# Kernel optimization log

Hardware: AMD Instinct MI355X
Metric: run time of the kernel (lower is better)

## Reference

```python
import jax, jax.numpy as jnp
import numpy as np

B, S, D, H = 4, 2048, 512, 8
DH = D // H  # 64


def setup_inputs() -> dict:
    key = jax.random.key(0)
    ks = jax.random.split(key, 12)
    sc = 0.02
    return {
        "embed": jax.random.normal(ks[0], (B, S, D), dtype=jnp.float32),
        "Wq": jax.random.normal(ks[1], (H, DH, D), dtype=jnp.float32) * sc,
        "bq": jax.random.normal(ks[2], (H, DH), dtype=jnp.float32) * sc,
        "Wk": jax.random.normal(ks[3], (H, DH, D), dtype=jnp.float32) * sc,
        "bk": jax.random.normal(ks[4], (H, DH), dtype=jnp.float32) * sc,
        "Wv": jax.random.normal(ks[5], (H, DH, D), dtype=jnp.float32) * sc,
        "bv": jax.random.normal(ks[6], (H, DH), dtype=jnp.float32) * sc,
        "Wo": jax.random.normal(ks[7], (D, D), dtype=jnp.float32) * sc,
        "bo": jax.random.normal(ks[8], (D,), dtype=jnp.float32) * sc,
        "gamma": jnp.ones((D,), dtype=jnp.float32),
        "beta": jnp.zeros((D,), dtype=jnp.float32),
    }


def reference(embed, Wq, bq, Wk, bk, Wv, bv, Wo, bo, gamma, beta):
    # Per-head linear projections, vectorized over heads: [B,H,S,DH]
    q = jnp.einsum("bsd,hed->bhse", embed, Wq) + bq[None, :, None, :]
    k = jnp.einsum("bsd,hed->bhse", embed, Wk) + bk[None, :, None, :]
    v = jnp.einsum("bsd,hed->bhse", embed, Wv) + bv[None, :, None, :]

    # Full score matrix [B,H,S,S], tril applied to RAW scores (zeros, not -inf),
    # scaled by sqrt(embedding_dim) -- faithful to the original module's math.
    att = jnp.einsum("bhse,bhte->bhst", q, k)
    att = jnp.tril(att)
    att = att / jnp.sqrt(jnp.float32(D))
    att = jax.nn.softmax(att, axis=-1)

    out = jnp.einsum("bhst,bhte->bhse", att, v)  # [B,H,S,DH]
    # concat heads along feature dim -> [B,S,D]
    out = jnp.transpose(out, (0, 2, 1, 3)).reshape(B, S, D)

    x = out @ Wo.T + bo
    x = x + embed

    # LayerNorm over last dim
    mu = jnp.mean(x, axis=-1, keepdims=True)
    var = jnp.var(x, axis=-1, keepdims=True)
    x = (x - mu) / jnp.sqrt(var + 1e-5) * gamma + beta
    return x
```

## Files before the change

### kernel.cpp

```cpp
#include <hip/hip_runtime.h>
#include <hip/hip_bf16.h>


typedef __bf16 bf16;
typedef __bf16 bf16x8 __attribute__((ext_vector_type(8)));
typedef __bf16 bf16x4v __attribute__((ext_vector_type(4)));
typedef float f32x4 __attribute__((ext_vector_type(4)));

#define S_LEN 2048
#define DMODEL 512
#define QSCALE 0.06375870914f

#define GLDS(g, l) __builtin_amdgcn_global_load_lds(                  \
    (const __attribute__((address_space(1))) void*)(g),               \
    (__attribute__((address_space(3))) void*)(l), 16, 0, 0)

__global__ __launch_bounds__(256) void cast_all(
    const float* __restrict__ embed, const float* __restrict__ Wq,
    const float* __restrict__ Wk, const float* __restrict__ Wv,
    const float* __restrict__ Wo,
    bf16* __restrict__ Eb, bf16* __restrict__ Wqkv, bf16* __restrict__ Wob) {
  int i = blockIdx.x * 256 + threadIdx.x;
  const float* src;
  bf16* dst;
  int il;
  if (i < 1048576) {
    src = embed; dst = Eb; il = i;
  } else {
    int j = i - 1048576;
    int w = j >> 16;
    il = j & 65535;
    src = (w == 0) ? Wq : (w == 1) ? Wk : (w == 2) ? Wv : Wo;
    dst = (w == 3) ? Wob : Wqkv + (size_t)w * 262144;
  }
  float4 v = reinterpret_cast<const float4*>(src)[il];
  bf16x4v o;
  o[0] = (bf16)v.x; o[1] = (bf16)v.y; o[2] = (bf16)v.z; o[3] = (bf16)v.w;
  *reinterpret_cast<bf16x4v*>(dst + (size_t)il * 4) = o;
}

__device__ __forceinline__ void gemm128_core(
    const bf16* __restrict__ A, const bf16* __restrict__ Bw,
    int row0, int col0, bf16* As, bf16* Bs, f32x4 (&acc)[4][4]) {
  int tid = threadIdx.x;
  int w = tid >> 6, l = tid & 63, lr = l & 15, lg = l >> 4;
  int wr = w >> 1, wc = w & 1;

  int srow = w * 8 + (l >> 3);
  int scol = ((l & 7) ^ (srow & 7)) << 3;
  const bf16* ga = A + (size_t)(row0 + srow) * DMODEL + scol;
  const bf16* gb = Bw + (size_t)(col0 + srow) * DMODEL + scol;
  char* asb = (char*)As;
  char* bsb = (char*)Bs;
  int sbase = w * 1024;

  int aoff[4], boff[4];
#pragma unroll
  for (int m = 0; m < 4; ++m) {
    aoff[m] = (wr * 64 + m * 16 + lr) * 128 + (((lg ^ (lr & 7))) << 4);
    boff[m] = (wc * 64 + m * 16 + lr) * 128 + (((lg ^ (lr & 7))) << 4);
  }

  for (int k0 = 0; k0 < DMODEL; k0 += 64) {
#pragma unroll
    for (int qt = 0; qt < 4; ++qt) {
      GLDS(ga + (size_t)qt * 32 * DMODEL, asb + qt * 4096 + sbase);
      GLDS(gb + (size_t)qt * 32 * DMODEL, bsb + qt * 4096 + sbase);
    }
    ga += 64; gb += 64;
    __syncthreads();

    bf16x8 af[2][4], bfv[2][4];
#pragma unroll
    for (int m = 0; m < 4; ++m) {
      af[0][m] = *(const bf16x8*)(asb + aoff[m]);
      af[1][m] = *(const bf16x8*)(asb + (aoff[m] ^ 0x40));
      bfv[0][m] = *(const bf16x8*)(bsb + boff[m]);
      bfv[1][m] = *(const bf16x8*)(bsb + (boff[m] ^ 0x40));
    }
#pragma unroll
    for (int m = 0; m < 4; ++m)
#pragma unroll
      for (int n = 0; n < 4; ++n) {
        acc[m][n] = __builtin_amdgcn_mfma_f32_16x16x32_bf16(af[0][m], bfv[0][n], acc[m][n], 0, 0, 0);
        acc[m][n] = __builtin_amdgcn_mfma_f32_16x16x32_bf16(af[1][m], bfv[1][n], acc[m][n], 0, 0, 0);
      }
    __syncthreads();
  }
}

__global__ __launch_bounds__(256) void gemm_qkv(
    const bf16* __restrict__ A, const bf16* __restrict__ Wqkv,
    const float* __restrict__ bq, const float* __restrict__ bk, const float* __restrict__ bv,
    bf16* __restrict__ Qb, bf16* __restrict__ Kb, bf16* __restrict__ Vt) {
  __shared__ __align__(16) bf16 As[128 * 64];
  __shared__ __align__(16) bf16 Bs[128 * 64];
  int row0 = blockIdx.x * 128, col0 = blockIdx.y * 128;
  f32x4 acc[4][4] = {};
  gemm128_core(A, Wqkv, row0, col0, As, Bs, acc);

  int tid = threadIdx.x;
  int w = tid >> 6, l = tid & 63, lr = l & 15, lg = l >> 4;
  int wr = w >> 1, wc = w & 1;
  int z2 = col0 >> 9;
  if (z2 < 2) {
    bf16* O = z2 ? Kb : Qb;
    const float* bias = z2 ? bk : bq;
    float qs = z2 ? 1.0f : QSCALE;
#pragma unroll
    for (int n = 0; n < 4; ++n) {
      int cg = (col0 & 511) + wc * 64 + n * 16 + lr;
      float bi = bias[cg];
#pragma unroll
      for (int m = 0; m < 4; ++m) {
        int rg = row0 + wr * 64 + m * 16 + lg * 4;
#pragma unroll
        for (int r = 0; r < 4; ++r)
          O[(size_t)(rg + r) * DMODEL + cg] = (bf16)((acc[m][n][r] + bi) * qs);
      }
    }
  } else {
#pragma unroll
    for (int n = 0; n < 4; ++n) {
      int ep = (col0 & 511) + wc * 64 + n * 16 + lr;
      int h = ep >> 6, e = ep & 63;
      float bi = bv[ep];
#pragma unroll
      for (int m = 0; m < 4; ++m) {
        int rg = row0 + wr * 64 + m * 16 + lg * 4;
        int b = rg >> 11, s0 = rg & 2047;
        bf16x4v pk;
#pragma unroll
        for (int r = 0; r < 4; ++r) pk[r] = (bf16)(acc[m][n][r] + bi);
        *(bf16x4v*)(Vt + ((size_t)((b * 8 + h) * 64 + e)) * S_LEN + s0) = pk;
      }
    }
  }
}

__global__ __launch_bounds__(256) void gemm_wo(
    const bf16* __restrict__ A, const bf16* __restrict__ W,
    const float* __restrict__ bo, const float* __restrict__ embed,
    bf16* __restrict__ X) {
  __shared__ __align__(16) bf16 As[128 * 64];
  __shared__ __align__(16) bf16 Bs[128 * 64];
  int row0 = blockIdx.x * 128, col0 = blockIdx.y * 128;
  f32x4 acc[4][4] = {};
  gemm128_core(A, W, row0, col0, As, Bs, acc);

  int tid = threadIdx.x;
  int w = tid >> 6, l = tid & 63, lr = l & 15, lg = l >> 4;
  int wr = w >> 1, wc = w & 1;
#pragma unroll
  for (int n = 0; n < 4; ++n) {
    int cg = col0 + wc * 64 + n * 16 + lr;
    float bi = bo[cg];
#pragma unroll
    for (int m = 0; m < 4; ++m) {
      int rg = row0 + wr * 64 + m * 16 + lg * 4;
#pragma unroll
      for (int r = 0; r < 4; ++r)
        X[(size_t)(rg + r) * DMODEL + cg] =
            (bf16)(acc[m][n][r] + bi + embed[(size_t)(rg + r) * DMODEL + cg]);
    }
  }
}

__global__ __launch_bounds__(512) void suf_kernel(const bf16* __restrict__ Vt,
                                                  float* __restrict__ SUF) {
  int bh = blockIdx.x;
  int e = threadIdx.x & 63;
  int seg = threadIdx.x >> 6;
  __shared__ float segtot[8][64];
  const bf16* vrow = Vt + ((size_t)bh * 64 + e) * S_LEN;
  float loc[16];
  float carry = 0.f;
#pragma unroll
  for (int j = 15; j >= 0; --j) {
    int jj = seg * 16 + j;
    bf16x8 a = *(const bf16x8*)(vrow + jj * 16);
    bf16x8 b2 = *(const bf16x8*)(vrow + jj * 16 + 8);
    float s = 0.f;
#pragma unroll
    for (int k = 0; k < 8; ++k) s += (float)a[k] + (float)b2[k];
    carry += s;
    loc[j] = carry;
  }
  segtot[seg][e] = carry;
  __syncthreads();
  float add = 0.f;
  for (int s2 = seg + 1; s2 < 8; ++s2) add += segtot[s2][e];
  float* srow = SUF + (size_t)bh * 129 * 64 + e;
#pragma unroll
  for (int j = 0; j < 16; ++j) srow[(size_t)(seg * 16 + j) * 64] = loc[j] + add;
  if (threadIdx.x < 64) srow[(size_t)128 * 64] = 0.f;
}

__global__ __launch_bounds__(512) void flash_attn(
    const bf16* __restrict__ Qb, const bf16* __restrict__ Kb,
    const bf16* __restrict__ Vt, const float* __restrict__ SUF,
    bf16* __restrict__ attO) {
  int bh = blockIdx.y;
  int b = bh >> 3, h = bh & 7;
  int p = (int)gridDim.x - 1 - (int)blockIdx.x;
  int tid = threadIdx.x;
  int w = tid >> 6, l = tid & 63, lr = l & 15, lg = l >> 4;
  int wsub = w & 3;
  int qtile = (w < 4) ? (16 + p) : (15 - p);
  int qb = qtile * 64;
  int nt = 17 + p;

  __shared__ __align__(16) bf16 kl[2][64 * 64];
  __shared__ __align__(16) bf16 vl[2][64 * 64];
  __shared__ __align__(16) bf16 pl[8][16 * 64];

  int srow = qb + 16 * wsub + lr;
  const bf16* qptr = Qb + ((size_t)(b * S_LEN) + srow) * DMODEL + h * 64 + lg * 8;
  bf16x8 aq0 = *(const bf16x8*)(qptr);
  bf16x8 aq1 = *(const bf16x8*)(qptr + 32);

  float lsum[4] = {0.f, 0.f, 0.f, 0.f};
  f32x4 acc[4] = {};

  int tmax_w = qb + 16 * wsub + 16;

  int grow = tid >> 3, gch = tid & 7;
  int sch = ((gch ^ (grow & 7)) << 3);
  const bf16* Kg = Kb + ((size_t)(b * S_LEN) + grow) * DMODEL + h * 64 + sch;
  const bf16* Vg = Vt + ((size_t)(bh * 64) + grow) * S_LEN + sch;
  int sdst = w * 1024;

  int sw0 = (lg ^ (lr & 7)) << 4;
  int sw4 = sw0 ^ 0x40;
  char* plb = (char*)pl[w];

  GLDS(Kg, (char*)kl[0] + sdst);
  GLDS(Vg, (char*)vl[0] + sdst);
  asm volatile("s_waitcnt vmcnt(0)" ::: "memory");
  __syncthreads();

  int cur = 0;
  for (int it = 0; it < nt; ++it) {
    int t0 = it << 6;
    if (it + 1 < nt) {
      GLDS(Kg + (size_t)(t0 + 64) * DMODEL, (char*)kl[cur ^ 1] + sdst);
      GLDS(Vg + (t0 + 64), (char*)vl[cur ^ 1] + sdst);
    }
    if (t0 < tmax_w) {
      char* klb = (char*)kl[cur];
      char* vlb = (char*)vl[cur];

      f32x4 sfrag[4];
      const f32x4 fz = {0.f, 0.f, 0.f, 0.f};
      __builtin_amdgcn_s_setprio(1);
#pragma unroll
      for (int c = 0; c < 4; ++c) {
        int rb = (16 * c + lr) * 128;
        bf16x8 bk0 = *(const bf16x8*)(klb + rb + sw0);
        bf16x8 bk1 = *(const bf16x8*)(klb + rb + sw4);
        f32x4 t = __builtin_amdgcn_mfma_f32_16x16x32_bf16(aq0, bk0, fz, 0, 0, 0);
        sfrag[c] = __builtin_amdgcn_mfma_f32_16x16x32_bf16(aq1, bk1, t, 0, 0, 0);
      }
      __builtin_amdgcn_s_setprio(0);

      if (t0 + 64 <= qb + 16 * wsub) {
#pragma unroll
        for (int r = 0; r < 4; ++r) {
          int row = lg * 4 + r;
          int pbase = row * 128 + ((lr & 7) << 1);
          int xorv = row & 7;
          float psum = 0.f;
#pragma unroll
          for (int c = 0; c < 4; ++c) {
            float pv = exp2f(sfrag[c][r]);
            psum += pv;
            int chunk = 2 * c + (lr >> 3);
            *(bf16*)(plb + pbase + (((chunk ^ xorv) << 4))) = (bf16)pv;
          }
          lsum[r] += psum;
        }
      } else {
#pragma unroll
        for (int r = 0; r < 4; ++r) {
          int sg = qb + 16 * wsub + lg * 4 + r;
          int row = lg * 4 + r;
          int pbase = row * 128 + ((lr & 7) << 1);
          int xorv = row & 7;
          float psum = 0.f;
#pragma unroll
          for (int c = 0; c < 4; ++c) {
            int tg = t0 + 16 * c + lr;
            float x = (tg <= sg) ? sfrag[c][r] : ((tg < tmax_w) ? 0.f : -1e30f);
            float pv = exp2f(x);
            psum += pv;
            int chunk = 2 * c + (lr >> 3);
            *(bf16*)(plb + pbase + (((chunk ^ xorv) << 4))) = (bf16)pv;
          }
          lsum[r] += psum;
        }
      }

      bf16x8 pa0 = *(const bf16x8*)(plb + lr * 128 + sw0);
      bf16x8 pa1 = *(const bf16x8*)(plb + lr * 128 + sw4);
      __builtin_amdgcn_s_setprio(1);
#pragma unroll
      for (int c = 0; c < 4; ++c) {
        int rb = (16 * c + lr) * 128;
        bf16x8 bv0 = *(const bf16x8*)(vlb + rb + sw0);
        bf16x8 bv1 = *(const bf16x8*)(vlb + rb + sw4);
        acc[c] = __builtin_amdgcn_mfma_f32_16x16x32_bf16(pa0, bv0, acc[c], 0, 0, 0);
        acc[c] = __builtin_amdgcn_mfma_f32_16x16x32_bf16(pa1, bv1, acc[c], 0, 0, 0);
      }
      __builtin_amdgcn_s_setprio(0);
    }
    asm volatile("s_waitcnt vmcnt(0)" ::: "memory");
    __syncthreads();
    cur ^= 1;
  }

#pragma unroll
  for (int r = 0; r < 4; ++r) {
#pragma unroll
    for (int d = 1; d < 16; d <<= 1) lsum[r] += __shfl_xor(lsum[r], d, 64);
  }

  int j16 = tmax_w >> 4;
  const float* suf = SUF + ((size_t)bh * 129 + j16) * 64;
  float cnt = (float)(S_LEN - tmax_w);
  float sufe[4];
#pragma unroll
  for (int c = 0; c < 4; ++c) sufe[c] = suf[16 * c + lr];
#pragma unroll
  for (int r = 0; r < 4; ++r) {
    float inv = 1.f / (lsum[r] + cnt);
    int sg = qb + 16 * wsub + lg * 4 + r;
#pragma unroll
    for (int c = 0; c < 4; ++c) {
      float o = (acc[c][r] + sufe[c]) * inv;
      attO[((size_t)(b * S_LEN) + sg) * DMODEL + h * 64 + 16 * c + lr] = (bf16)o;
    }
  }
}

__global__ __launch_bounds__(256) void ln_kernel(const bf16* __restrict__ x,
                                                 const float* __restrict__ gamma,
                                                 const float* __restrict__ beta,
                                                 float* __restrict__ out) {
  int row = blockIdx.x * 4 + (threadIdx.x >> 6);
  int l = threadIdx.x & 63;
  bf16x8 xv = *(const bf16x8*)(x + (size_t)row * DMODEL + l * 8);
  float xf[8];
  float s = 0.f, s2 = 0.f;
#pragma unroll
  for (int k = 0; k < 8; ++k) {
    xf[k] = (float)xv[k];
    s += xf[k];
    s2 += xf[k] * xf[k];
  }
#pragma unroll
  for (int d = 1; d < 64; d <<= 1) {
    s += __shfl_xor(s, d, 64);
    s2 += __shfl_xor(s2, d, 64);
  }
  float mean = s * (1.f / 512.f);
  float var = s2 * (1.f / 512.f) - mean * mean;
  float rstd = rsqrtf(var + 1e-5f);
  const float4* g4 = reinterpret_cast<const float4*>(gamma) + l * 2;
  const float4* b4 = reinterpret_cast<const float4*>(beta) + l * 2;
  float4 g0 = g4[0], g1 = g4[1], bb0 = b4[0], bb1 = b4[1];
  float4 o0, o1;
  o0.x = (xf[0] - mean) * rstd * g0.x + bb0.x;
  o0.y = (xf[1] - mean) * rstd * g0.y + bb0.y;
  o0.z = (xf[2] - mean) * rstd * g0.z + bb0.z;
  o0.w = (xf[3] - mean) * rstd * g0.w + bb0.w;
  o1.x = (xf[4] - mean) * rstd * g1.x + bb1.x;
  o1.y = (xf[5] - mean) * rstd * g1.y + bb1.y;
  o1.z = (xf[6] - mean) * rstd * g1.z + bb1.z;
  o1.w = (xf[7] - mean) * rstd * g1.w + bb1.w;
  float4* orow = reinterpret_cast<float4*>(out + (size_t)row * DMODEL) + l * 2;
  orow[0] = o0;
  orow[1] = o1;
}

extern "C" void kernel_launch(void* const* d_in, const int* in_sizes, int n_in,
                              void* d_out, int out_size, void* d_ws, size_t ws_size,
                              hipStream_t stream) {
  const float* embed = (const float*)d_in[0];
  const float* Wq = (const float*)d_in[1];
  const float* bq = (const float*)d_in[2];
  const float* Wk = (const float*)d_in[3];
  const float* bk = (const float*)d_in[4];
  const float* Wv = (const float*)d_in[5];
  const float* bv = (const float*)d_in[6];
  const float* Wo = (const float*)d_in[7];
  const float* bo = (const float*)d_in[8];
  const float* gamma = (const float*)d_in[9];
  const float* beta = (const float*)d_in[10];
  float* out = (float*)d_out;

  char* ws = (char*)d_ws;
  size_t off = 0;
  auto alc = [&](size_t b) { size_t o = off; off += (b + 255) & ~(size_t)255; return o; };
  bf16* Eb    = (bf16*)(ws + alc(8192ull * 512 * 2));
  bf16* Wqkv  = (bf16*)(ws + alc(1536ull * 512 * 2));
  bf16* Wob   = (bf16*)(ws + alc(512ull * 512 * 2));
  bf16* Qb    = (bf16*)(ws + alc(8192ull * 512 * 2));
  bf16* Kb    = (bf16*)(ws + alc(8192ull * 512 * 2));
  bf16* Vt    = (bf16*)(ws + alc(8192ull * 512 * 2));
  float* SUF  = (float*)(ws + alc(32ull * 129 * 64 * 4));
  bf16* AttO  = (bf16*)(ws + alc(8192ull * 512 * 2));
  bf16* Xb    = (bf16*)(ws + alc(8192ull * 512 * 2));
  (void)ws_size; (void)n_in; (void)in_sizes; (void)out_size;

  cast_all<<<5120, 256, 0, stream>>>(embed, Wq, Wk, Wv, Wo, Eb, Wqkv, Wob);

  gemm_qkv<<<dim3(64, 12), 256, 0, stream>>>(Eb, Wqkv, bq, bk, bv, Qb, Kb, Vt);
  suf_kernel<<<32, 512, 0, stream>>>(Vt, SUF);
  flash_attn<<<dim3(16, 32), 512, 0, stream>>>(Qb, Kb, Vt, SUF, AttO);
  gemm_wo<<<dim3(64, 4), 256, 0, stream>>>(AttO, Wob, bo, embed, Xb);
  ln_kernel<<<2048, 256, 0, stream>>>(Xb, gamma, beta, out);
}
```

Measured before the change: 111.3 us.

## Use 32x32x16 MFMA with register-resident P via permlane swaps in attention

Rewrites the flash attention inner loop to compute S^T with 32x32x16 MFMAs, so each wave owns 32 query rows. The P matrix now stays in registers, rearranged with v_permlane32_swap, which removes the per-wave LDS staging of P and the extra LDS round trips. Blocks are reassigned so each handles 4 pairs of 32-row tiles (front and back) over 8 x-blocks, with per-wave early cutoff and diagonal masking at 32-row granularity. The row sums are reduced through a small shared array for output normalisation. The cost is fewer blocks and more accumulator registers per wave.

```diff
diff --git a/kernel.cpp b/kernel.cpp
--- a/kernel.cpp
+++ b/kernel.cpp
@@ -5,7 +5,11 @@
 typedef __bf16 bf16;
 typedef __bf16 bf16x8 __attribute__((ext_vector_type(8)));
 typedef __bf16 bf16x4v __attribute__((ext_vector_type(4)));
+typedef __bf16 bf16x2 __attribute__((ext_vector_type(2)));
 typedef float f32x4 __attribute__((ext_vector_type(4)));
+typedef float f32x16 __attribute__((ext_vector_type(16)));
+typedef unsigned int u32;
+typedef u32 u32x4 __attribute__((ext_vector_type(4)));
 
 #define S_LEN 2048
 #define DMODEL 512
@@ -14,6 +18,8 @@
 #define GLDS(g, l) __builtin_amdgcn_global_load_lds(                  \
     (const __attribute__((address_space(1))) void*)(g),               \
     (__attribute__((address_space(3))) void*)(l), 16, 0, 0)
+
+#define PSWAP(a, b) asm volatile("v_permlane32_swap_b32 %0, %1" : "+v"(a), "+v"(b))
 
 __global__ __launch_bounds__(256) void cast_all(
     const float* __restrict__ embed, const float* __restrict__ Wq,
@@ -196,33 +202,54 @@
   if (threadIdx.x < 64) srow[(size_t)128 * 64] = 0.f;
 }
 
+__device__ __forceinline__ void softmax_pack(const f32x16& sf, bool diag, int lh,
+                                             int ls, float& lsum, u32* w8) {
+#pragma unroll
+  for (int i = 0; i < 8; ++i) {
+    float x0 = sf[2 * i], x1 = sf[2 * i + 1];
+    if (diag) {
+      int t0 = ((2 * i) & 3) + 8 * (i >> 1) + 4 * lh;
+      x0 = (t0 <= ls) ? x0 : 0.f;
+      x1 = (t0 + 1 <= ls) ? x1 : 0.f;
+    }
+    float e0 = exp2f(x0), e1 = exp2f(x1);
+    lsum += e0 + e1;
+    bf16x2 pk;
+    pk[0] = (bf16)e0; pk[1] = (bf16)e1;
+    w8[i] = __builtin_bit_cast(u32, pk);
+  }
+}
+
 __global__ __launch_bounds__(512) void flash_attn(
     const bf16* __restrict__ Qb, const bf16* __restrict__ Kb,
     const bf16* __restrict__ Vt, const float* __restrict__ SUF,
     bf16* __restrict__ attO) {
   int bh = blockIdx.y;
   int b = bh >> 3, h = bh & 7;
-  int p = (int)gridDim.x - 1 - (int)blockIdx.x;
+  int p = blockIdx.x;
   int tid = threadIdx.x;
-  int w = tid >> 6, l = tid & 63, lr = l & 15, lg = l >> 4;
+  int w = tid >> 6, l = tid & 63, lh = l >> 5, ls = l & 31;
+
+  int pe = (w >> 2) ? (p + 8) : p;
   int wsub = w & 3;
-  int qtile = (w < 4) ? (16 + p) : (15 - p);
-  int qb = qtile * 64;
-  int nt = 17 + p;
+  int qt32 = (wsub < 2) ? (32 + 2 * pe + wsub) : (31 - 2 * pe - (wsub - 2));
+  int qb_w = qt32 * 32;
+  int tmax_w = qb_w + 32;
+  int nt_w = (tmax_w + 63) >> 6;
+  int nt = 25 + p;
+  int dsub = (qb_w >> 5) & 1;
 
   __shared__ __align__(16) bf16 kl[2][64 * 64];
   __shared__ __align__(16) bf16 vl[2][64 * 64];
-  __shared__ __align__(16) bf16 pl[8][16 * 64];
-
-  int srow = qb + 16 * wsub + lr;
-  const bf16* qptr = Qb + ((size_t)(b * S_LEN) + srow) * DMODEL + h * 64 + lg * 8;
-  bf16x8 aq0 = *(const bf16x8*)(qptr);
-  bf16x8 aq1 = *(const bf16x8*)(qptr + 32);
-
-  float lsum[4] = {0.f, 0.f, 0.f, 0.f};
-  f32x4 acc[4] = {};
-
-  int tmax_w = qb + 16 * wsub + 16;
+  __shared__ float lsumS[8][32];
+
+  const bf16* qrow = Qb + ((size_t)(b * S_LEN) + qb_w + ls) * DMODEL + h * 64 + lh * 8;
+  bf16x8 qf[4];
+#pragma unroll
+  for (int ki = 0; ki < 4; ++ki) qf[ki] = *(const bf16x8*)(qrow + ki * 16);
+
+  f32x16 acc0 = {}, acc1 = {};
+  float lsum = 0.f;
 
   int grow = tid >> 3, gch = tid & 7;
   int sch = ((gch ^ (grow & 7)) << 3);
@@ -230,9 +257,10 @@
   const bf16* Vg = Vt + ((size_t)(bh * 64) + grow) * S_LEN + sch;
   int sdst = w * 1024;
 
-  int sw0 = (lg ^ (lr & 7)) << 4;
-  int sw4 = sw0 ^ 0x40;
-  char* plb = (char*)pl[w];
+  int cx[4];
+#pragma unroll
+  for (int ki = 0; ki < 4; ++ki) cx[ki] = (((2 * ki + lh) ^ (ls & 7)) << 4);
+  int rb = ls * 128;
 
   GLDS(Kg, (char*)kl[0] + sdst);
   GLDS(Vg, (char*)vl[0] + sdst);
@@ -241,104 +269,90 @@
 
   int cur = 0;
   for (int it = 0; it < nt; ++it) {
-    int t0 = it << 6;
     if (it + 1 < nt) {
-      GLDS(Kg + (size_t)(t0 + 64) * DMODEL, (char*)kl[cur ^ 1] + sdst);
-      GLDS(Vg + (t0 + 64), (char*)vl[cur ^ 1] + sdst);
-    }
-    if (t0 < tmax_w) {
+      int t1 = (it + 1) << 6;
+      GLDS(Kg + (size_t)t1 * DMODEL, (char*)kl[cur ^ 1] + sdst);
+      GLDS(Vg + t1, (char*)vl[cur ^ 1] + sdst);
+    }
+    if (it < nt_w) {
       char* klb = (char*)kl[cur];
       char* vlb = (char*)vl[cur];
-
-      f32x4 sfrag[4];
-      const f32x4 fz = {0.f, 0.f, 0.f, 0.f};
-      __builtin_amdgcn_s_setprio(1);
-#pragma unroll
-      for (int c = 0; c < 4; ++c) {
-        int rb = (16 * c + lr) * 128;
-        bf16x8 bk0 = *(const bf16x8*)(klb + rb + sw0);
-        bf16x8 bk1 = *(const bf16x8*)(klb + rb + sw4);
-        f32x4 t = __builtin_amdgcn_mfma_f32_16x16x32_bf16(aq0, bk0, fz, 0, 0, 0);
-        sfrag[c] = __builtin_amdgcn_mfma_f32_16x16x32_bf16(aq1, bk1, t, 0, 0, 0);
-      }
-      __builtin_amdgcn_s_setprio(0);
-
-      if (t0 + 64 <= qb + 16 * wsub) {
-#pragma unroll
-        for (int r = 0; r < 4; ++r) {
-          int row = lg * 4 + r;
-          int pbase = row * 128 + ((lr & 7) << 1);
-          int xorv = row & 7;
-          float psum = 0.f;
-#pragma unroll
-          for (int c = 0; c < 4; ++c) {
-            float pv = exp2f(sfrag[c][r]);
-            psum += pv;
-            int chunk = 2 * c + (lr >> 3);
-            *(bf16*)(plb + pbase + (((chunk ^ xorv) << 4))) = (bf16)pv;
-          }
-          lsum[r] += psum;
+      bool last = (it == nt_w - 1);
+      int nsub = (last && dsub == 0) ? 1 : 2;
+
+      f32x16 sf0 = {}, sf1 = {};
+#pragma unroll
+      for (int ki = 0; ki < 4; ++ki) {
+        bf16x8 ka = *(const bf16x8*)(klb + rb + cx[ki]);
+        sf0 = __builtin_amdgcn_mfma_f32_32x32x16_bf16(ka, qf[ki], sf0, 0, 0, 0);
+      }
+      if (nsub == 2) {
+#pragma unroll
+        for (int ki = 0; ki < 4; ++ki) {
+          bf16x8 ka = *(const bf16x8*)(klb + rb + 32 * 128 + cx[ki]);
+          sf1 = __builtin_amdgcn_mfma_f32_32x32x16_bf16(ka, qf[ki], sf1, 0, 0, 0);
         }
-      } else {
-#pragma unroll
-        for (int r = 0; r < 4; ++r) {
-          int sg = qb + 16 * wsub + lg * 4 + r;
-          int row = lg * 4 + r;
-          int pbase = row * 128 + ((lr & 7) << 1);
-          int xorv = row & 7;
-          float psum = 0.f;
-#pragma unroll
-          for (int c = 0; c < 4; ++c) {
-            int tg = t0 + 16 * c + lr;
-            float x = (tg <= sg) ? sfrag[c][r] : ((tg < tmax_w) ? 0.f : -1e30f);
-            float pv = exp2f(x);
-            psum += pv;
-            int chunk = 2 * c + (lr >> 3);
-            *(bf16*)(plb + pbase + (((chunk ^ xorv) << 4))) = (bf16)pv;
-          }
-          lsum[r] += psum;
-        }
-      }
-
-      bf16x8 pa0 = *(const bf16x8*)(plb + lr * 128 + sw0);
-      bf16x8 pa1 = *(const bf16x8*)(plb + lr * 128 + sw4);
-      __builtin_amdgcn_s_setprio(1);
-#pragma unroll
-      for (int c = 0; c < 4; ++c) {
-        int rb = (16 * c + lr) * 128;
-        bf16x8 bv0 = *(const bf16x8*)(vlb + rb + sw0);
-        bf16x8 bv1 = *(const bf16x8*)(vlb + rb + sw4);
-        acc[c] = __builtin_amdgcn_mfma_f32_16x16x32_bf16(pa0, bv0, acc[c], 0, 0, 0);
-        acc[c] = __builtin_amdgcn_mfma_f32_16x16x32_bf16(pa1, bv1, acc[c], 0, 0, 0);
-      }
-      __builtin_amdgcn_s_setprio(0);
+      }
+
+      u32 pw[16];
+      softmax_pack(sf0, last && (dsub == 0), lh, ls, lsum, pw);
+      PSWAP(pw[0], pw[2]); PSWAP(pw[1], pw[3]);
+      PSWAP(pw[4], pw[6]); PSWAP(pw[5], pw[7]);
+      if (nsub == 2) {
+        softmax_pack(sf1, last && (dsub == 1), lh, ls, lsum, pw + 8);
+        PSWAP(pw[8], pw[10]); PSWAP(pw[9], pw[11]);
+        PSWAP(pw[12], pw[14]); PSWAP(pw[13], pw[15]);
+      }
+
+      u32x4 f0v = {pw[0], pw[1], pw[2], pw[3]};
+      u32x4 f1v = {pw[4], pw[5], pw[6], pw[7]};
+      bf16x8 pa0 = __builtin_bit_cast(bf16x8, f0v);
+      bf16x8 pa1 = __builtin_bit_cast(bf16x8, f1v);
+      {
+        bf16x8 v00 = *(const bf16x8*)(vlb + rb + cx[0]);
+        bf16x8 v01 = *(const bf16x8*)(vlb + rb + cx[1]);
+        bf16x8 v10 = *(const bf16x8*)(vlb + rb + 32 * 128 + cx[0]);
+        bf16x8 v11 = *(const bf16x8*)(vlb + rb + 32 * 128 + cx[1]);
+        acc0 = __builtin_amdgcn_mfma_f32_32x32x16_bf16(pa0, v00, acc0, 0, 0, 0);
+        acc0 = __builtin_amdgcn_mfma_f32_32x32x16_bf16(pa1, v01, acc0, 0, 0, 0);
+        acc1 = __builtin_amdgcn_mfma_f32_32x32x16_bf16(pa0, v10, acc1, 0, 0, 0);
+        acc1 = __builtin_amdgcn_mfma_f32_32x32x16_bf16(pa1, v11, acc1, 0, 0, 0);
+      }
+      if (nsub == 2) {
+        u32x4 f2v = {pw[8], pw[9], pw[10], pw[11]};
+        u32x4 f3v = {pw[12], pw[13], pw[14], pw[15]};
+        bf16x8 pa2 = __builtin_bit_cast(bf16x8, f2v);
+        bf16x8 pa3 = __builtin_bit_cast(bf16x8, f3v);
+        bf16x8 v02 = *(const bf16x8*)(vlb + rb + cx[2]);
+        bf16x8 v03 = *(const bf16x8*)(vlb + rb + cx[3]);
+        bf16x8 v12 = *(const bf16x8*)(vlb + rb + 32 * 128 + cx[2]);
+        bf16x8 v13 = *(const bf16x8*)(vlb + rb + 32 * 128 + cx[3]);
+        acc0 = __builtin_amdgcn_mfma_f32_32x32x16_bf16(pa2, v02, acc0, 0, 0, 0);
+        acc0 = __builtin_amdgcn_mfma_f32_32x32x16_bf16(pa3, v03, acc0, 0, 0, 0);
+        acc1 = __builtin_amdgcn_mfma_f32_32x32x16_bf16(pa2, v12, acc1, 0, 0, 0);
+        acc1 = __builtin_amdgcn_mfma_f32_32x32x16_bf16(pa3, v13, acc1, 0, 0, 0);
+      }
     }
     asm volatile("s_waitcnt vmcnt(0)" ::: "memory");
     __syncthreads();
     cur ^= 1;
   }
 
-#pragma unroll
-  for (int r = 0; r < 4; ++r) {
-#pragma unroll
-    for (int d = 1; d < 16; d <<= 1) lsum[r] += __shfl_xor(lsum[r], d, 64);
-  }
+  lsum += __shfl_xor(lsum, 32, 64);
+  lsumS[w][ls] = lsum;
 
   int j16 = tmax_w >> 4;
   const float* suf = SUF + ((size_t)bh * 129 + j16) * 64;
   float cnt = (float)(S_LEN - tmax_w);
-  float sufe[4];
-#pragma unroll
-  for (int c = 0; c < 4; ++c) sufe[c] = suf[16 * c + lr];
-#pragma unroll
-  for (int r = 0; r < 4; ++r) {
-    float inv = 1.f / (lsum[r] + cnt);
-    int sg = qb + 16 * wsub + lg * 4 + r;
-#pragma unroll
-    for (int c = 0; c < 4; ++c) {
-      float o = (acc[c][r] + sufe[c]) * inv;
-      attO[((size_t)(b * S_LEN) + sg) * DMODEL + h * 64 + 16 * c + lr] = (bf16)o;
-    }
+  float suf0 = suf[ls], suf1 = suf[ls + 32];
+
+  bf16* obase = attO + ((size_t)(b * S_LEN) + qb_w) * DMODEL + h * 64 + ls;
+#pragma unroll
+  for (int r = 0; r < 16; ++r) {
+    int sr = (r & 3) + 8 * (r >> 2) + 4 * lh;
+    float inv = 1.f / (lsumS[w][sr] + cnt);
+    obase[(size_t)sr * DMODEL] = (bf16)((acc0[r] + suf0) * inv);
+    obase[(size_t)sr * DMODEL + 32] = (bf16)((acc1[r] + suf1) * inv);
   }
 }
 
@@ -416,7 +430,7 @@
 
   gemm_qkv<<<dim3(64, 12), 256, 0, stream>>>(Eb, Wqkv, bq, bk, bv, Qb, Kb, Vt);
   suf_kernel<<<32, 512, 0, stream>>>(Vt, SUF);
-  flash_attn<<<dim3(16, 32), 512, 0, stream>>>(Qb, Kb, Vt, SUF, AttO);
+  flash_attn<<<dim3(8, 32), 512, 0, stream>>>(Qb, Kb, Vt, SUF, AttO);
   gemm_wo<<<dim3(64, 4), 256, 0, stream>>>(AttO, Wob, bo, embed, Xb);
   ln_kernel<<<2048, 256, 0, stream>>>(Xb, gamma, beta, out);
 }
```

Measured after the change: 128.3 us. 15.3% more time.

## Fuse embed bf16 cast into QKV GEMM and widen suffix-sum kernel grid

Applied to the files above, without the earlier changes.

The QKV GEMM now reads embed as fp32 straight from global memory into registers, converts it to bf16 and writes it into the swizzled LDS tile, with the next tile's loads prefetched in software. This removes the separate cast pass over embed and its bf16 workspace buffer, so embed is read once and no intermediate is written. The weight cast becomes its own small 2D-grid kernel. The suffix-sum kernel is split across 256 blocks of 256 threads instead of 32 blocks, to spread the work over more CUs, at the cost of a longer shared-memory reduction per thread.

```diff
diff --git a/kernel.cpp b/kernel.cpp
--- a/kernel.cpp
+++ b/kernel.cpp
@@ -15,28 +15,138 @@
     (const __attribute__((address_space(1))) void*)(g),               \
     (__attribute__((address_space(3))) void*)(l), 16, 0, 0)
 
-__global__ __launch_bounds__(256) void cast_all(
-    const float* __restrict__ embed, const float* __restrict__ Wq,
-    const float* __restrict__ Wk, const float* __restrict__ Wv,
-    const float* __restrict__ Wo,
-    bf16* __restrict__ Eb, bf16* __restrict__ Wqkv, bf16* __restrict__ Wob) {
+__global__ __launch_bounds__(256) void cast_w(
+    const float* __restrict__ a0, const float* __restrict__ a1,
+    const float* __restrict__ a2, const float* __restrict__ a3,
+    bf16* __restrict__ o0, bf16* __restrict__ o1,
+    bf16* __restrict__ o2, bf16* __restrict__ o3) {
+  int y = blockIdx.y;
+  const float* in = (y == 0) ? a0 : (y == 1) ? a1 : (y == 2) ? a2 : a3;
+  bf16* out = (y == 0) ? o0 : (y == 1) ? o1 : (y == 2) ? o2 : o3;
   int i = blockIdx.x * 256 + threadIdx.x;
-  const float* src;
-  bf16* dst;
-  int il;
-  if (i < 1048576) {
-    src = embed; dst = Eb; il = i;
-  } else {
-    int j = i - 1048576;
-    int w = j >> 16;
-    il = j & 65535;
-    src = (w == 0) ? Wq : (w == 1) ? Wk : (w == 2) ? Wv : Wo;
-    dst = (w == 3) ? Wob : Wqkv + (size_t)w * 262144;
-  }
-  float4 v = reinterpret_cast<const float4*>(src)[il];
+  float4 v = reinterpret_cast<const float4*>(in)[i];
   bf16x4v o;
   o[0] = (bf16)v.x; o[1] = (bf16)v.y; o[2] = (bf16)v.z; o[3] = (bf16)v.w;
-  *reinterpret_cast<bf16x4v*>(dst + (size_t)il * 4) = o;
+  *reinterpret_cast<bf16x4v*>(out + (size_t)i * 4) = o;
+}
+
+__global__ __launch_bounds__(256) void gemm_qkv(
+    const float* __restrict__ Af32, const bf16* __restrict__ Wqkv,
+    const float* __restrict__ bq, const float* __restrict__ bk, const float* __restrict__ bv,
+    bf16* __restrict__ Qb, bf16* __restrict__ Kb, bf16* __restrict__ Vt) {
+  __shared__ __align__(16) bf16 As[128 * 64];
+  __shared__ __align__(16) bf16 Bs[128 * 64];
+  int row0 = blockIdx.x * 128, col0 = blockIdx.y * 128;
+  int tid = threadIdx.x;
+  int w = tid >> 6, l = tid & 63, lr = l & 15, lg = l >> 4;
+  int wr = w >> 1, wc = w & 1;
+
+  int srow = w * 8 + (l >> 3);
+  int scol = ((l & 7) ^ (srow & 7)) << 3;
+  const bf16* gb = Wqkv + (size_t)(col0 + srow) * DMODEL + scol;
+  char* asb = (char*)As;
+  char* bsb = (char*)Bs;
+  int sbase = w * 1024;
+
+  int ac = l & 7;
+  const float* ga = Af32 + (size_t)(row0 + srow) * DMODEL + ac * 8;
+  int awoff = srow * 128 + ((ac ^ (srow & 7)) << 4);
+
+  int aoff[4], boff[4];
+#pragma unroll
+  for (int m = 0; m < 4; ++m) {
+    aoff[m] = (wr * 64 + m * 16 + lr) * 128 + (((lg ^ (lr & 7))) << 4);
+    boff[m] = (wc * 64 + m * 16 + lr) * 128 + (((lg ^ (lr & 7))) << 4);
+  }
+
+  f32x4 acc[4][4] = {};
+  float4 ar[4][2];
+#pragma unroll
+  for (int u = 0; u < 4; ++u) {
+    ar[u][0] = *(const float4*)(ga + (size_t)u * 32 * DMODEL);
+    ar[u][1] = *(const float4*)(ga + (size_t)u * 32 * DMODEL + 4);
+  }
+
+  for (int k0 = 0; k0 < DMODEL; k0 += 64) {
+#pragma unroll
+    for (int qt = 0; qt < 4; ++qt)
+      GLDS(gb + (size_t)qt * 32 * DMODEL, bsb + qt * 4096 + sbase);
+    gb += 64;
+
+#pragma unroll
+    for (int u = 0; u < 4; ++u) {
+      bf16x8 av;
+      av[0] = (bf16)ar[u][0].x; av[1] = (bf16)ar[u][0].y;
+      av[2] = (bf16)ar[u][0].z; av[3] = (bf16)ar[u][0].w;
+      av[4] = (bf16)ar[u][1].x; av[5] = (bf16)ar[u][1].y;
+      av[6] = (bf16)ar[u][1].z; av[7] = (bf16)ar[u][1].w;
+      *(bf16x8*)(asb + u * 4096 + awoff) = av;
+    }
+    ga += 64;
+    if (k0 + 64 < DMODEL) {
+#pragma unroll
+      for (int u = 0; u < 4; ++u) {
+        ar[u][0] = *(const float4*)(ga + (size_t)u * 32 * DMODEL);
+        ar[u][1] = *(const float4*)(ga + (size_t)u * 32 * DMODEL + 4);
+      }
+      asm volatile("s_waitcnt vmcnt(8)" ::: "memory");
+    } else {
+      asm volatile("s_waitcnt vmcnt(0)" ::: "memory");
+    }
+    __syncthreads();
+
+    bf16x8 af[2][4], bfv[2][4];
+#pragma unroll
+    for (int m = 0; m < 4; ++m) {
+      af[0][m] = *(const bf16x8*)(asb + aoff[m]);
+      af[1][m] = *(const bf16x8*)(asb + (aoff[m] ^ 0x40));
+      bfv[0][m] = *(const bf16x8*)(bsb + boff[m]);
+      bfv[1][m] = *(const bf16x8*)(bsb + (boff[m] ^ 0x40));
+    }
+#pragma unroll
+    for (int m = 0; m < 4; ++m)
+#pragma unroll
+      for (int n = 0; n < 4; ++n) {
+        acc[m][n] = __builtin_amdgcn_mfma_f32_16x16x32_bf16(af[0][m], bfv[0][n], acc[m][n], 0, 0, 0);
+        acc[m][n] = __builtin_amdgcn_mfma_f32_16x16x32_bf16(af[1][m], bfv[1][n], acc[m][n], 0, 0, 0);
+      }
+    __syncthreads();
+  }
+
+  int z2 = col0 >> 9;
+  if (z2 < 2) {
+    bf16* O = z2 ? Kb : Qb;
+    const float* bias = z2 ? bk : bq;
+    float qs = z2 ? 1.0f : QSCALE;
+#pragma unroll
+    for (int n = 0; n < 4; ++n) {
+      int cg = (col0 & 511) + wc * 64 + n * 16 + lr;
+      float bi = bias[cg];
+#pragma unroll
+      for (int m = 0; m < 4; ++m) {
+        int rg = row0 + wr * 64 + m * 16 + lg * 4;
+#pragma unroll
+        for (int r = 0; r < 4; ++r)
+          O[(size_t)(rg + r) * DMODEL + cg] = (bf16)((acc[m][n][r] + bi) * qs);
+      }
+    }
+  } else {
+#pragma unroll
+    for (int n = 0; n < 4; ++n) {
+      int ep = (col0 & 511) + wc * 64 + n * 16 + lr;
+      int h = ep >> 6, e = ep & 63;
+      float bi = bv[ep];
+#pragma unroll
+      for (int m = 0; m < 4; ++m) {
+        int rg = row0 + wr * 64 + m * 16 + lg * 4;
+        int b = rg >> 11, s0 = rg & 2047;
+        bf16x4v pk;
+#pragma unroll
+        for (int r = 0; r < 4; ++r) pk[r] = (bf16)(acc[m][n][r] + bi);
+        *(bf16x4v*)(Vt + ((size_t)((b * 8 + h) * 64 + e)) * S_LEN + s0) = pk;
+      }
+    }
+  }
 }
 
 __device__ __forceinline__ void gemm128_core(
@@ -86,55 +196,6 @@
         acc[m][n] = __builtin_amdgcn_mfma_f32_16x16x32_bf16(af[1][m], bfv[1][n], acc[m][n], 0, 0, 0);
       }
     __syncthreads();
-  }
-}
-
-__global__ __launch_bounds__(256) void gemm_qkv(
-    const bf16* __restrict__ A, const bf16* __restrict__ Wqkv,
-    const float* __restrict__ bq, const float* __restrict__ bk, const float* __restrict__ bv,
-    bf16* __restrict__ Qb, bf16* __restrict__ Kb, bf16* __restrict__ Vt) {
-  __shared__ __align__(16) bf16 As[128 * 64];
-  __shared__ __align__(16) bf16 Bs[128 * 64];
-  int row0 = blockIdx.x * 128, col0 = blockIdx.y * 128;
-  f32x4 acc[4][4] = {};
-  gemm128_core(A, Wqkv, row0, col0, As, Bs, acc);
-
-  int tid = threadIdx.x;
-  int w = tid >> 6, l = tid & 63, lr = l & 15, lg = l >> 4;
-  int wr = w >> 1, wc = w & 1;
-  int z2 = col0 >> 9;
-  if (z2 < 2) {
-    bf16* O = z2 ? Kb : Qb;
-    const float* bias = z2 ? bk : bq;
-    float qs = z2 ? 1.0f : QSCALE;
-#pragma unroll
-    for (int n = 0; n < 4; ++n) {
-      int cg = (col0 & 511) + wc * 64 + n * 16 + lr;
-      float bi = bias[cg];
-#pragma unroll
-      for (int m = 0; m < 4; ++m) {
-        int rg = row0 + wr * 64 + m * 16 + lg * 4;
-#pragma unroll
-        for (int r = 0; r < 4; ++r)
-          O[(size_t)(rg + r) * DMODEL + cg] = (bf16)((acc[m][n][r] + bi) * qs);
-      }
-    }
-  } else {
-#pragma unroll
-    for (int n = 0; n < 4; ++n) {
-      int ep = (col0 & 511) + wc * 64 + n * 16 + lr;
-      int h = ep >> 6, e = ep & 63;
-      float bi = bv[ep];
-#pragma unroll
-      for (int m = 0; m < 4; ++m) {
-        int rg = row0 + wr * 64 + m * 16 + lg * 4;
-        int b = rg >> 11, s0 = rg & 2047;
-        bf16x4v pk;
-#pragma unroll
-        for (int r = 0; r < 4; ++r) pk[r] = (bf16)(acc[m][n][r] + bi);
-        *(bf16x4v*)(Vt + ((size_t)((b * 8 + h) * 64 + e)) * S_LEN + s0) = pk;
-      }
-    }
   }
 }
 
@@ -166,18 +227,20 @@
   }
 }
 
-__global__ __launch_bounds__(512) void suf_kernel(const bf16* __restrict__ Vt,
+__global__ __launch_bounds__(256) void suf_kernel(const bf16* __restrict__ Vt,
                                                   float* __restrict__ SUF) {
-  int bh = blockIdx.x;
-  int e = threadIdx.x & 63;
-  int seg = threadIdx.x >> 6;
-  __shared__ float segtot[8][64];
+  int bh = blockIdx.x >> 3;
+  int eg = blockIdx.x & 7;
+  int el = threadIdx.x & 7;
+  int seg = threadIdx.x >> 3;
+  int e = eg * 8 + el;
+  __shared__ float segtot[32][9];
   const bf16* vrow = Vt + ((size_t)bh * 64 + e) * S_LEN;
-  float loc[16];
+  float loc[4];
   float carry = 0.f;
 #pragma unroll
-  for (int j = 15; j >= 0; --j) {
-    int jj = seg * 16 + j;
+  for (int j = 3; j >= 0; --j) {
+    int jj = seg * 4 + j;
     bf16x8 a = *(const bf16x8*)(vrow + jj * 16);
     bf16x8 b2 = *(const bf16x8*)(vrow + jj * 16 + 8);
     float s = 0.f;
@@ -186,14 +249,14 @@
     carry += s;
     loc[j] = carry;
   }
-  segtot[seg][e] = carry;
+  segtot[seg][el] = carry;
   __syncthreads();
   float add = 0.f;
-  for (int s2 = seg + 1; s2 < 8; ++s2) add += segtot[s2][e];
+  for (int s2 = seg + 1; s2 < 32; ++s2) add += segtot[s2][el];
   float* srow = SUF + (size_t)bh * 129 * 64 + e;
 #pragma unroll
-  for (int j = 0; j < 16; ++j) srow[(size_t)(seg * 16 + j) * 64] = loc[j] + add;
-  if (threadIdx.x < 64) srow[(size_t)128 * 64] = 0.f;
+  for (int j = 0; j < 4; ++j) srow[(size_t)(seg * 4 + j) * 64] = loc[j] + add;
+  if (seg == 0) srow[(size_t)128 * 64] = 0.f;
 }
 
 __global__ __launch_bounds__(512) void flash_attn(
@@ -401,7 +464,6 @@
   char* ws = (char*)d_ws;
   size_t off = 0;
   auto alc = [&](size_t b) { size_t o = off; off += (b + 255) & ~(size_t)255; return o; };
-  bf16* Eb    = (bf16*)(ws + alc(8192ull * 512 * 2));
   bf16* Wqkv  = (bf16*)(ws + alc(1536ull * 512 * 2));
   bf16* Wob   = (bf16*)(ws + alc(512ull * 512 * 2));
   bf16* Qb    = (bf16*)(ws + alc(8192ull * 512 * 2));
@@ -412,10 +474,11 @@
   bf16* Xb    = (bf16*)(ws + alc(8192ull * 512 * 2));
   (void)ws_size; (void)n_in; (void)in_sizes; (void)out_size;
 
-  cast_all<<<5120, 256, 0, stream>>>(embed, Wq, Wk, Wv, Wo, Eb, Wqkv, Wob);
-
-  gemm_qkv<<<dim3(64, 12), 256, 0, stream>>>(Eb, Wqkv, bq, bk, bv, Qb, Kb, Vt);
-  suf_kernel<<<32, 512, 0, stream>>>(Vt, SUF);
+  cast_w<<<dim3(256, 4), 256, 0, stream>>>(
+      Wq, Wk, Wv, Wo, Wqkv, Wqkv + 512ull * 512, Wqkv + 1024ull * 512, Wob);
+
+  gemm_qkv<<<dim3(64, 12), 256, 0, stream>>>(embed, Wqkv, bq, bk, bv, Qb, Kb, Vt);
+  suf_kernel<<<256, 256, 0, stream>>>(Vt, SUF);
   flash_attn<<<dim3(16, 32), 512, 0, stream>>>(Qb, Kb, Vt, SUF, AttO);
   gemm_wo<<<dim3(64, 4), 256, 0, stream>>>(AttO, Wob, bo, embed, Xb);
   ln_kernel<<<2048, 256, 0, stream>>>(Xb, gamma, beta, out);
```

New measurement: 112.5 us. About the same (+1.1%).
